# Performance work log

Hardware: AMD Instinct MI355X
Metric: run time of the kernel (lower is better)

## Reference

```python
import jax, jax.numpy as jnp
import numpy as np
import math

D_MODEL = 1024
N_HEADS = 16
D_HEAD = D_MODEL // N_HEADS
EPS = 1e-5


def layer_norm(x, w, b):
    mu = jnp.mean(x, axis=-1, keepdims=True)
    var = jnp.mean(jnp.square(x - mu), axis=-1, keepdims=True)
    return (x - mu) * jax.lax.rsqrt(var + EPS) * w + b


def setup_inputs() -> dict:
    key = jax.random.key(0)
    ks = jax.random.split(key, 8)
    b, n, d = 1, 4096, D_MODEL
    s = 0.02
    return {
        "x": jax.random.normal(ks[0], (b, n, d), dtype=jnp.float32),
        "ln1_w": jnp.ones((d,), jnp.float32),
        "ln1_b": jnp.zeros((d,), jnp.float32),
        "ln2_w": jnp.ones((d,), jnp.float32),
        "ln2_b": jnp.zeros((d,), jnp.float32),
        "w_qkv": jax.random.normal(ks[1], (d, 3 * d), jnp.float32) * s,  # [in, out]
        "w_o": jax.random.normal(ks[2], (d, d), jnp.float32) * s,
        "w_ff1": jax.random.normal(ks[3], (d, 4 * d), jnp.float32) * s,
        "b_ff1": jnp.zeros((4 * d,), jnp.float32),
        "w_ff2": jax.random.normal(ks[4], (4 * d, d), jnp.float32) * s,
        "b_ff2": jnp.zeros((d,), jnp.float32),
    }


def reference(x, ln1_w, ln1_b, ln2_w, ln2_b, w_qkv, w_o, w_ff1, b_ff1, w_ff2, b_ff2):
    b, n, d = x.shape
    # --- attention sub-block ---
    h = layer_norm(x, ln1_w, ln1_b)
    qkv = (h @ w_qkv).reshape(b, n, 3, N_HEADS, D_HEAD)
    q, k, v = qkv[:, :, 0], qkv[:, :, 1], qkv[:, :, 2]  # [b, n, h, dh]
    scale = 1.0 / math.sqrt(D_HEAD)
    s = jnp.einsum("bqhd,bkhd->bhqk", q, k) * scale  # materialized [b,h,n,n]
    causal = jnp.tril(jnp.ones((n, n), dtype=bool))
    s = jnp.where(causal, s, -jnp.inf)
    a = jax.nn.softmax(s, axis=-1)
    out = jnp.einsum("bhqk,bkhd->bqhd", a, v).reshape(b, n, d)
    x = x + out @ w_o
    # --- FFN sub-block ---
    h2 = layer_norm(x, ln2_w, ln2_b)
    ff = jax.nn.gelu(h2 @ w_ff1 + b_ff1, approximate=False) @ w_ff2 + b_ff2
    return x + ff
```

## Files before the change

kernel.cpp:

```cpp
#include <hip/hip_runtime.h>
#include <hip/hip_bf16.h>
#include <cstdint>
#include <cstddef>

typedef __attribute__((ext_vector_type(8))) __bf16 bf16x8;
typedef __attribute__((ext_vector_type(4))) __bf16 bf16x4;
typedef __attribute__((ext_vector_type(4))) float f32x4;
typedef __attribute__((ext_vector_type(16))) float f32x16;
typedef __attribute__((ext_vector_type(4))) unsigned int uint4v;

#define MFMA16(a, b, c) __builtin_amdgcn_mfma_f32_16x16x32_bf16(a, b, c, 0, 0, 0)
#define MFMA32(a, b, c) __builtin_amdgcn_mfma_f32_32x32x16_bf16(a, b, c, 0, 0, 0)

__device__ __forceinline__ void gload_lds16(const void* g, void* l) {
  __builtin_amdgcn_global_load_lds(
      (__attribute__((address_space(1))) uint32_t*)g,
      (__attribute__((address_space(3))) uint32_t*)l,
      16, 0, 0);
}

__device__ __forceinline__ unsigned pkbf(float a, float b) {
  unsigned short x = __builtin_bit_cast(unsigned short, (__bf16)a);
  unsigned short y = __builtin_bit_cast(unsigned short, (__bf16)b);
  return (unsigned)x | ((unsigned)y << 16);
}

__global__ __launch_bounds__(256) void transpose_all_kernel(
    const float* __restrict__ w_qkv, __bf16* __restrict__ wqkvT,
    const float* __restrict__ w_o, __bf16* __restrict__ woT,
    const float* __restrict__ w_ff1, __bf16* __restrict__ wff1T,
    const float* __restrict__ w_ff2, __bf16* __restrict__ wff2T) {
  __shared__ float tile[32][33];
  int bid = blockIdx.x;
  const float* in; __bf16* out; int K, N, bx, by;
  if (bid < 3072)      { in = w_qkv; out = wqkvT; K = 1024; N = 3072; bx = bid % 96;  by = bid / 96; }
  else if (bid < 4096) { int b = bid - 3072; in = w_o;   out = woT;   K = 1024; N = 1024; bx = b % 32;  by = b / 32; }
  else if (bid < 8192) { int b = bid - 4096; in = w_ff1; out = wff1T; K = 1024; N = 4096; bx = b % 128; by = b / 128; }
  else                 { int b = bid - 8192; in = w_ff2; out = wff2T; K = 4096; N = 1024; bx = b % 32;  by = b / 32; }
  int tx = threadIdx.x, ty = threadIdx.y;
  int gcol = bx * 32 + tx;
#pragma unroll
  for (int j = 0; j < 4; j++) {
    int grow = by * 32 + ty + j * 8;
    tile[ty + j * 8][tx] = in[(size_t)grow * N + gcol];
  }
  __syncthreads();
#pragma unroll
  for (int j = 0; j < 4; j++) {
    int n = bx * 32 + ty + j * 8;
    out[(size_t)n * K + by * 32 + tx] = (__bf16)tile[tx][ty + j * 8];
  }
}

__global__ __launch_bounds__(256) void ln_kernel(
    const float* __restrict__ x, const float* __restrict__ w,
    const float* __restrict__ b, __bf16* __restrict__ out) {
  int row = blockIdx.x;
  int t = threadIdx.x;
  const float4* xr = (const float4*)(x + (size_t)row * 1024);
  float4 v = xr[t];
  float s = v.x + v.y + v.z + v.w;
  float sq = v.x * v.x + v.y * v.y + v.z * v.z + v.w * v.w;
#pragma unroll
  for (int m = 1; m < 64; m <<= 1) {
    s += __shfl_xor(s, m);
    sq += __shfl_xor(sq, m);
  }
  __shared__ float rs[4], rq[4];
  int wid = t >> 6;
  if ((t & 63) == 0) { rs[wid] = s; rq[wid] = sq; }
  __syncthreads();
  s = rs[0] + rs[1] + rs[2] + rs[3];
  sq = rq[0] + rq[1] + rq[2] + rq[3];
  float mean = s * (1.0f / 1024.0f);
  float var = sq * (1.0f / 1024.0f) - mean * mean;
  float rstd = rsqrtf(var + 1e-5f);
  int c = t * 4;
  float4 wv = ((const float4*)w)[t];
  float4 bv = ((const float4*)b)[t];
  bf16x4 o;
  o[0] = (__bf16)((v.x - mean) * rstd * wv.x + bv.x);
  o[1] = (__bf16)((v.y - mean) * rstd * wv.y + bv.y);
  o[2] = (__bf16)((v.z - mean) * rstd * wv.z + bv.z);
  o[3] = (__bf16)((v.w - mean) * rstd * wv.w + bv.w);
  *(bf16x4*)(out + (size_t)row * 1024 + c) = o;
}

template <int EPI>
__global__ __launch_bounds__(256, 2) void gemm_kernel(
    const __bf16* __restrict__ A, const __bf16* __restrict__ BT,
    int M, int N, int K,
    const float* __restrict__ resid, const float* __restrict__ bias,
    float* __restrict__ outf, __bf16* __restrict__ outb) {
  __shared__ __bf16 lsA[128 * 64];
  __shared__ __bf16 lsB[128 * 64];
  int t = threadIdx.x;
  int m0 = blockIdx.y * 128, n0 = blockIdx.x * 128;
  int wid = t >> 6, lane = t & 63, lo = lane & 15, g = lane >> 4;
  int wr = wid >> 1, wc = wid & 1;
  f32x4 acc[4][4] = {};
  const __bf16* ag = A + (size_t)(m0 + (t >> 3)) * K + (t & 7) * 8;
  const __bf16* bg = BT + (size_t)(n0 + (t >> 3)) * K + (t & 7) * 8;
  for (int k0 = 0; k0 < K; k0 += 64) {
#pragma unroll
    for (int i = 0; i < 4; i++) {
      gload_lds16(ag + (size_t)i * 32 * K + k0, &lsA[i * 2048 + t * 8]);
      gload_lds16(bg + (size_t)i * 32 * K + k0, &lsB[i * 2048 + t * 8]);
    }
    __syncthreads();
#pragma unroll
    for (int kk = 0; kk < 2; kk++) {
      bf16x8 af[4], bfr[4];
#pragma unroll
      for (int mi = 0; mi < 4; mi++)
        af[mi] = *(const bf16x8*)&lsA[(wr * 64 + mi * 16 + lo) * 64 + kk * 32 + g * 8];
#pragma unroll
      for (int ni = 0; ni < 4; ni++)
        bfr[ni] = *(const bf16x8*)&lsB[(wc * 64 + ni * 16 + lo) * 64 + kk * 32 + g * 8];
#pragma unroll
      for (int mi = 0; mi < 4; mi++)
#pragma unroll
        for (int ni = 0; ni < 4; ni++)
          acc[mi][ni] = MFMA16(af[mi], bfr[ni], acc[mi][ni]);
    }
    __syncthreads();
  }
#pragma unroll
  for (int mi = 0; mi < 4; mi++) {
#pragma unroll
    for (int ni = 0; ni < 4; ni++) {
      int col = n0 + wc * 64 + ni * 16 + lo;
      int row0 = m0 + wr * 64 + mi * 16 + g * 4;
#pragma unroll
      for (int r = 0; r < 4; r++) {
        int row = row0 + r;
        float val = acc[mi][ni][r];
        size_t idx = (size_t)row * N + col;
        outf[idx] = resid[idx] + val;
      }
    }
  }
}

template <int EPI>
__global__ __launch_bounds__(512, 2) void gemm256_kernel(
    const __bf16* __restrict__ A, const __bf16* __restrict__ BT,
    int M, int N, int K, int nkc,
    const float* __restrict__ bias, __bf16* __restrict__ outb,
    __bf16* __restrict__ P0, __bf16* __restrict__ P1,
    __bf16* __restrict__ P2, __bf16* __restrict__ P3) {
  __shared__ __bf16 lsA[2][2][128 * 64];
  __shared__ __bf16 lsB[2][2][128 * 64];
  int nbx = N >> 8;
  int nwg = (M >> 8) * nbx;
  int bid = blockIdx.x;
  int swz = (bid & 7) * (nwg >> 3) + (bid >> 3);
  int m0 = (swz / nbx) << 8, n0 = (swz % nbx) << 8;
  int kc = blockIdx.y;
  int kt0 = kc * nkc;
  int t = threadIdx.x;
  int wid = t >> 6, lane = t & 63, lo = lane & 15, g = lane >> 4;
  int wm = wid >> 2, wn = wid & 3;
  int srow = t >> 3, sgrp = t & 7;

  auto stA = [&](int d, int h, int kt) {
#pragma unroll
    for (int i = 0; i < 2; i++) {
      int row = i * 64 + srow;
      int gs = (sgrp ^ (row & 7)) * 8;
      gload_lds16(A + (size_t)(m0 + h * 128 + row) * K + kt * 64 + gs,
                  &lsA[d][h][(i * 512 + t) * 8]);
    }
  };
  auto stB = [&](int d, int h, int kt) {
#pragma unroll
    for (int i = 0; i < 2; i++) {
      int row = i * 64 + srow;
      int gs = (sgrp ^ (row & 7)) * 8;
      gload_lds16(BT + (size_t)(n0 + h * 128 + row) * K + kt * 64 + gs,
                  &lsB[d][h][(i * 512 + t) * 8]);
    }
  };
  auto rdA = [&](int d, int f, int kk) -> bf16x8 {
    int row = (f & 3) * 32 + wm * 16 + lo;
    return *(const bf16x8*)&lsA[d][f >> 2][row * 64 + (((kk * 4 + g) ^ (lo & 7)) * 8)];
  };
  auto rdB = [&](int d, int ni, int kk) -> bf16x8 {
    int row = (ni & 1) * 64 + wn * 16 + lo;
    return *(const bf16x8*)&lsB[d][ni >> 1][row * 64 + (((kk * 4 + g) ^ (lo & 7)) * 8)];
  };

  f32x4 acc[8][4] = {};
  stA(0, 0, kt0); stB(0, 0, kt0); stB(0, 1, kt0); stA(0, 1, kt0);
  asm volatile("s_waitcnt vmcnt(4)" ::: "memory");
  __builtin_amdgcn_s_barrier();

  for (int ki = 0; ki < nkc; ki++) {
    int kt = kt0 + ki;
    int d = ki & 1, nx = d ^ 1;
    bool pf = (ki + 1) < nkc;
    bf16x8 fa[4][2], fb0[2][2], fb1[2][2];
#pragma unroll
    for (int f = 0; f < 4; f++) { fa[f][0] = rdA(d, f, 0); fa[f][1] = rdA(d, f, 1); }
#pragma unroll
    for (int n = 0; n < 2; n++) { fb0[n][0] = rdB(d, n, 0); fb0[n][1] = rdB(d, n, 1); }
    if (pf) { stA(nx, 0, kt + 1); stB(nx, 0, kt + 1); }
    __builtin_amdgcn_s_barrier();
    __builtin_amdgcn_s_setprio(1);
#pragma unroll
    for (int f = 0; f < 4; f++)
#pragma unroll
      for (int n = 0; n < 2; n++) {
        acc[f][n] = MFMA16(fa[f][0], fb0[n][0], acc[f][n]);
        acc[f][n] = MFMA16(fa[f][1], fb0[n][1], acc[f][n]);
      }
    __builtin_amdgcn_s_setprio(0);
    asm volatile("s_waitcnt vmcnt(6)" ::: "memory");
    __builtin_amdgcn_s_barrier();
#pragma unroll
    for (int n = 0; n < 2; n++) { fb1[n][0] = rdB(d, 2 + n, 0); fb1[n][1] = rdB(d, 2 + n, 1); }
    if (pf) stB(nx, 1, kt + 1);
    __builtin_amdgcn_s_barrier();
    __builtin_amdgcn_s_setprio(1);
#pragma unroll
    for (int f = 0; f < 4; f++)
#pragma unroll
      for (int n = 0; n < 2; n++) {
        acc[f][2 + n] = MFMA16(fa[f][0], fb1[n][0], acc[f][2 + n]);
        acc[f][2 + n] = MFMA16(fa[f][1], fb1[n][1], acc[f][2 + n]);
      }
    __builtin_amdgcn_s_setprio(0);
    asm volatile("s_waitcnt vmcnt(6)" ::: "memory");
    __builtin_amdgcn_s_barrier();
#pragma unroll
    for (int f = 0; f < 4; f++) { fa[f][0] = rdA(d, 4 + f, 0); fa[f][1] = rdA(d, 4 + f, 1); }
    if (pf) stA(nx, 1, kt + 1);
    __builtin_amdgcn_s_barrier();
    __builtin_amdgcn_s_setprio(1);
#pragma unroll
    for (int f = 0; f < 4; f++)
#pragma unroll
      for (int n = 0; n < 2; n++) {
        acc[4 + f][2 + n] = MFMA16(fa[f][0], fb1[n][0], acc[4 + f][2 + n]);
        acc[4 + f][2 + n] = MFMA16(fa[f][1], fb1[n][1], acc[4 + f][2 + n]);
      }
    __builtin_amdgcn_s_setprio(0);
    __builtin_amdgcn_s_barrier();
    __builtin_amdgcn_s_setprio(1);
#pragma unroll
    for (int f = 0; f < 4; f++)
#pragma unroll
      for (int n = 0; n < 2; n++) {
        acc[4 + f][n] = MFMA16(fa[f][0], fb0[n][0], acc[4 + f][n]);
        acc[4 + f][n] = MFMA16(fa[f][1], fb0[n][1], acc[4 + f][n]);
      }
    __builtin_amdgcn_s_setprio(0);
    asm volatile("s_waitcnt vmcnt(4)" ::: "memory");
    __builtin_amdgcn_s_barrier();
  }

  __bf16* pk = (EPI == 4) ? ((kc == 0) ? P0 : (kc == 1) ? P1 : (kc == 2) ? P2 : P3)
                          : nullptr;
#pragma unroll
  for (int f = 0; f < 8; f++) {
    int row0 = m0 + (f >> 2) * 128 + (f & 3) * 32 + wm * 16 + g * 4;
#pragma unroll
    for (int ni = 0; ni < 4; ni++) {
      int col = n0 + (ni >> 1) * 128 + (ni & 1) * 64 + wn * 16 + lo;
      if (EPI == 0) {
        int sE = col >> 10, rem = col & 1023, hh = rem >> 6, dd = rem & 63;
        if (sE < 2) {
          float qs = (sE == 0) ? 0.1803368801111204f : 1.0f;
#pragma unroll
          for (int r = 0; r < 4; r++)
            outb[((size_t)(sE * 16 + hh) * 4096 + row0 + r) * 64 + dd] =
                (__bf16)(acc[f][ni][r] * qs);
        } else {
          bf16x4 pk4;
#pragma unroll
          for (int r = 0; r < 4; r++) pk4[r] = (__bf16)acc[f][ni][r];
          *(bf16x4*)&outb[(size_t)32 * 4096 * 64 + ((size_t)(hh * 64 + dd)) * 4096 + row0] = pk4;
        }
      } else if (EPI == 2) {
        float bv = bias[col];
#pragma unroll
        for (int r = 0; r < 4; r++) {
          float vv = acc[f][ni][r] + bv;
          float gg = 0.5f * vv * (1.0f + erff(vv * 0.70710678118f));
          outb[(size_t)(row0 + r) * N + col] = (__bf16)gg;
        }
      } else {
#pragma unroll
        for (int r = 0; r < 4; r++)
          pk[(size_t)(row0 + r) * N + col] = (__bf16)acc[f][ni][r];
      }
    }
  }
}

__global__ __launch_bounds__(256) void ff2_reduce_kernel(
    const __bf16* __restrict__ p0, const __bf16* __restrict__ p1,
    const __bf16* __restrict__ p2, const __bf16* __restrict__ p3,
    const float* __restrict__ x2, const float* __restrict__ bias,
    float* __restrict__ out) {
  size_t i8 = ((size_t)blockIdx.x * 256 + threadIdx.x) * 8;
  bf16x8 a = *(const bf16x8*)&p0[i8];
  bf16x8 b = *(const bf16x8*)&p1[i8];
  bf16x8 c = *(const bf16x8*)&p2[i8];
  bf16x8 d = *(const bf16x8*)&p3[i8];
  int col = (int)(i8 & 1023);
  float4 xa = *(const float4*)&x2[i8];
  float4 xb = *(const float4*)&x2[i8 + 4];
  float4 ba = *(const float4*)&bias[col];
  float4 bb = *(const float4*)&bias[col + 4];
  float4 oa, ob;
  oa.x = xa.x + ba.x + (float)a[0] + (float)b[0] + (float)c[0] + (float)d[0];
  oa.y = xa.y + ba.y + (float)a[1] + (float)b[1] + (float)c[1] + (float)d[1];
  oa.z = xa.z + ba.z + (float)a[2] + (float)b[2] + (float)c[2] + (float)d[2];
  oa.w = xa.w + ba.w + (float)a[3] + (float)b[3] + (float)c[3] + (float)d[3];
  ob.x = xb.x + bb.x + (float)a[4] + (float)b[4] + (float)c[4] + (float)d[4];
  ob.y = xb.y + bb.y + (float)a[5] + (float)b[5] + (float)c[5] + (float)d[5];
  ob.z = xb.z + bb.z + (float)a[6] + (float)b[6] + (float)c[6] + (float)d[6];
  ob.w = xb.w + bb.w + (float)a[7] + (float)b[7] + (float)c[7] + (float)d[7];
  *(float4*)&out[i8] = oa;
  *(float4*)&out[i8 + 4] = ob;
}

__global__ __launch_bounds__(512, 4) void attn_kernel(
    const __bf16* __restrict__ Q, const __bf16* __restrict__ Kb,
    const __bf16* __restrict__ VTb, __bf16* __restrict__ O) {
  constexpr int NSEQ = 4096;
  __shared__ __bf16 lds[2][2][2][64 * 64];
  int orig = blockIdx.x;
  int xcd = orig & 7, rank = orig >> 3;
  int hv = rank >> 5;
  int hd2 = (rank >> 4) & 1;
  int itr = rank & 15;
  int head = xcd * 2 + hd2;
  int it = hv ? itr : (31 - itr);
  int t = threadIdx.x, wid = t >> 6, lane = t & 63;
  int lo = lane & 31, hi = lane >> 5;
  int qsub = wid & 3, kpar = wid >> 2;
  const __bf16* kh = Kb + (size_t)head * NSEQ * 64;
  const __bf16* vth = VTb + (size_t)head * 64 * NSEQ;
  int qlow = it * 128 + qsub * 32;
  int qrow = qlow + lo;
  const __bf16* qh = Q + (size_t)head * NSEQ * 64 + (size_t)qrow * 64;
  bf16x8 bq[4];
#pragma unroll
  for (int c = 0; c < 4; c++) bq[c] = *(const bf16x8*)(qh + c * 16 + hi * 8);

  const unsigned onesu = 0x3F803F80u;
  uint4v onev = {onesu, onesu, onesu, onesu};
  bf16x8 vones = __builtin_bit_cast(bf16x8, onev);

  f32x16 acc0 = {}, acc1 = {};
  f32x16 lacc = {};
  int srow = t >> 3;
  int sgs = ((t & 7) ^ (srow & 7)) * 8;

  auto stage_tile = [&](int d, int par, int kt) {
    gload_lds16(kh + (size_t)(kt * 64 + srow) * 64 + sgs, &lds[d][par][0][t * 8]);
    gload_lds16(vth + (size_t)srow * NSEQ + kt * 64 + sgs, &lds[d][par][1][t * 8]);
  };

  int ns = it + 1;
  stage_tile(0, 0, 0);
  stage_tile(0, 1, 1);
  __syncthreads();
  for (int j = 0; j < ns; j++) {
    int cur = j & 1;
    if (j + 1 < ns) {
      stage_tile(cur ^ 1, 0, 2 * j + 2);
      stage_tile(cur ^ 1, 1, 2 * j + 3);
    }
    int kt = 2 * j + kpar;
    if (kt * 64 <= qlow + 31) {
      const __bf16* lk = lds[cur][kpar][0];
      const __bf16* lvt = lds[cur][kpar][1];
      f32x16 s0 = {}, s1 = {};
      __builtin_amdgcn_s_setprio(1);
#pragma unroll
      for (int c = 0; c < 4; c++) {
        bf16x8 ka0 = *(const bf16x8*)&lk[(size_t)lo * 64 + (((c * 2 + hi) ^ (lo & 7)) * 8)];
        bf16x8 ka1 = *(const bf16x8*)&lk[(size_t)(32 + lo) * 64 + (((c * 2 + hi) ^ (lo & 7)) * 8)];
        s0 = MFMA32(ka0, bq[c], s0);
        s1 = MFMA32(ka1, bq[c], s1);
      }
      __builtin_amdgcn_s_setprio(0);
      if (kt * 64 + 63 > qlow) {
#pragma unroll
        for (int i = 0; i < 16; i++) {
          int key0 = kt * 64 + (i & 3) + 8 * (i >> 2) + 4 * hi;
          if (key0 > qrow) s0[i] = -3.0e38f;
          if (key0 + 32 > qrow) s1[i] = -3.0e38f;
        }
      }
#pragma unroll
      for (int i = 0; i < 16; i++) {
        s0[i] = exp2f(s0[i]);
        s1[i] = exp2f(s1[i]);
      }
      uint4v pw[4];
#pragma unroll
      for (int b = 0; b < 2; b++) {
        int off = b * 8;
        unsigned a0 = pkbf(s0[off + 0], s0[off + 1]);
        unsigned a1 = pkbf(s0[off + 2], s0[off + 3]);
        unsigned b0 = pkbf(s0[off + 4], s0[off + 5]);
        unsigned b1 = pkbf(s0[off + 6], s0[off + 7]);
        asm("v_permlane32_swap_b32 %0, %1" : "+v"(a0), "+v"(b0));
        asm("v_permlane32_swap_b32 %0, %1" : "+v"(a1), "+v"(b1));
        pw[b][0] = a0; pw[b][1] = a1; pw[b][2] = b0; pw[b][3] = b1;
        unsigned c0 = pkbf(s1[off + 0], s1[off + 1]);
        unsigned c1 = pkbf(s1[off + 2], s1[off + 3]);
        unsigned d0 = pkbf(s1[off + 4], s1[off + 5]);
        unsigned d1 = pkbf(s1[off + 6], s1[off + 7]);
        asm("v_permlane32_swap_b32 %0, %1" : "+v"(c0), "+v"(d0));
        asm("v_permlane32_swap_b32 %0, %1" : "+v"(c1), "+v"(d1));
        pw[2 + b][0] = c0; pw[2 + b][1] = c1; pw[2 + b][2] = d0; pw[2 + b][3] = d1;
      }
      __builtin_amdgcn_s_setprio(1);
#pragma unroll
      for (int b = 0; b < 4; b++) {
        bf16x8 pf = __builtin_bit_cast(bf16x8, pw[b]);
        bf16x8 va0 = *(const bf16x8*)&lvt[(size_t)lo * 64 + (((b * 2 + hi) ^ (lo & 7)) * 8)];
        bf16x8 va1 = *(const bf16x8*)&lvt[(size_t)(32 + lo) * 64 + (((b * 2 + hi) ^ (lo & 7)) * 8)];
        acc0 = MFMA32(va0, pf, acc0);
        acc1 = MFMA32(va1, pf, acc1);
        lacc = MFMA32(vones, pf, lacc);
      }
      __builtin_amdgcn_s_setprio(0);
    }
    __syncthreads();
  }
  float* fl = (float*)lds;
  float* lbuf = fl;
  float* ab = fl + 256;
  __bf16* bounce = (__bf16*)(fl + 256 + 9216);
  if (kpar == 1) {
    lbuf[qsub * 64 + lane] = lacc[0];
    int base = (qsub * 64 + lane) * 36;
#pragma unroll
    for (int k2 = 0; k2 < 16; k2 += 4) {
      float4 v0; v0.x = acc0[k2]; v0.y = acc0[k2 + 1]; v0.z = acc0[k2 + 2]; v0.w = acc0[k2 + 3];
      *(float4*)&ab[base + k2] = v0;
      float4 v1; v1.x = acc1[k2]; v1.y = acc1[k2 + 1]; v1.z = acc1[k2 + 2]; v1.w = acc1[k2 + 3];
      *(float4*)&ab[base + 16 + k2] = v1;
    }
  }
  __syncthreads();
  if (kpar == 0) {
    float lsum = lacc[0] + lbuf[qsub * 64 + lane];
    float linv = 1.0f / lsum;
    int base = (qsub * 64 + lane) * 36;
    f32x16 b0, b1;
#pragma unroll
    for (int k2 = 0; k2 < 16; k2 += 4) {
      float4 v0 = *(float4*)&ab[base + k2];
      b0[k2] = v0.x; b0[k2 + 1] = v0.y; b0[k2 + 2] = v0.z; b0[k2 + 3] = v0.w;
      float4 v1 = *(float4*)&ab[base + 16 + k2];
      b1[k2] = v1.x; b1[k2 + 1] = v1.y; b1[k2 + 2] = v1.z; b1[k2 + 3] = v1.w;
    }
    __bf16* region = bounce + qsub * 2048;
#pragma unroll
    for (int dt = 0; dt < 2; dt++) {
#pragma unroll
      for (int rp = 0; rp < 8; rp++) {
        int r = rp * 2;
        float a0 = dt ? acc1[r] : acc0[r], a1 = dt ? acc1[r + 1] : acc0[r + 1];
        float c0 = dt ? b1[r] : b0[r], c1 = dt ? b1[r + 1] : b0[r + 1];
        float e0 = (a0 + c0) * linv;
        float e1 = (a1 + c1) * linv;
        int d = dt * 32 + (r & 3) + 8 * (r >> 2) + 4 * hi;
        int bytecol = d * 2;
        int g16 = bytecol >> 4, rem16 = bytecol & 15;
        *(unsigned*)((char*)region + lo * 128 + ((g16 ^ (lo & 7)) * 16 + rem16)) = pkbf(e0, e1);
      }
    }
#pragma unroll
    for (int j2 = 0; j2 < 4; j2++) {
      int idx = j2 * 64 + lane;
      int row = idx >> 3, g = idx & 7;
      bf16x8 v = *(const bf16x8*)((char*)region + row * 128 + ((g ^ (row & 7)) * 16));
      *(bf16x8*)&O[(size_t)(it * 128 + qsub * 32 + row) * 1024 + head * 64 + g * 8] = v;
    }
  }
}

extern "C" void kernel_launch(void* const* d_in, const int* in_sizes, int n_in,
                              void* d_out, int out_size, void* d_ws, size_t ws_size,
                              hipStream_t stream) {
  const float* x = (const float*)d_in[0];
  const float* ln1_w = (const float*)d_in[1];
  const float* ln1_b = (const float*)d_in[2];
  const float* ln2_w = (const float*)d_in[3];
  const float* ln2_b = (const float*)d_in[4];
  const float* w_qkv = (const float*)d_in[5];
  const float* w_o = (const float*)d_in[6];
  const float* w_ff1 = (const float*)d_in[7];
  const float* b_ff1 = (const float*)d_in[8];
  const float* w_ff2 = (const float*)d_in[9];
  const float* b_ff2 = (const float*)d_in[10];
  float* out = (float*)d_out;

  const size_t D = 1024, NT = 4096;
  __bf16* wqkvT = (__bf16*)d_ws;
  __bf16* woT = wqkvT + 3072 * D;
  __bf16* wff1T = woT + D * D;
  __bf16* wff2T = wff1T + 4096 * D;
  __bf16* hbuf = wff2T + D * 4096;
  __bf16* qkvb = hbuf + NT * D;
  __bf16* attnb = qkvb + 3 * NT * D;
  __bf16* a1 = qkvb;
  float* x2 = (float*)(attnb + NT * D);
  __bf16* p0 = (__bf16*)d_ws;
  __bf16* p1 = p0 + NT * D;
  __bf16* p2 = hbuf;
  __bf16* p3 = (__bf16*)(x2 + NT * D);

  dim3 tb(32, 8);
  transpose_all_kernel<<<12288, tb, 0, stream>>>(w_qkv, wqkvT, w_o, woT,
                                                 w_ff1, wff1T, w_ff2, wff2T);

  ln_kernel<<<4096, 256, 0, stream>>>(x, ln1_w, ln1_b, hbuf);
  gemm256_kernel<0><<<192, 512, 0, stream>>>(hbuf, wqkvT, 4096, 3072, 1024, 16,
                                             nullptr, qkvb, nullptr, nullptr, nullptr, nullptr);
  attn_kernel<<<512, 512, 0, stream>>>(
      qkvb, qkvb + 16 * NT * 64, qkvb + 32 * NT * 64, attnb);
  gemm_kernel<1><<<dim3(1024 / 128, 4096 / 128), 256, 0, stream>>>(
      attnb, woT, 4096, 1024, 1024, x, nullptr, x2, nullptr);
  ln_kernel<<<4096, 256, 0, stream>>>(x2, ln2_w, ln2_b, hbuf);
  gemm256_kernel<2><<<256, 512, 0, stream>>>(hbuf, wff1T, 4096, 4096, 1024, 16,
                                             b_ff1, a1, nullptr, nullptr, nullptr, nullptr);
  gemm256_kernel<4><<<dim3(64, 4), 512, 0, stream>>>(a1, wff2T, 4096, 1024, 4096, 16,
                                                     nullptr, nullptr, p0, p1, p2, p3);
  ff2_reduce_kernel<<<2048, 256, 0, stream>>>(p0, p1, p2, p3, x2, b_ff2, out);
}
```

Baseline: 247.8 us.

## Split-K the output projection GEMM and unroll attention loop by buffer parity

The output projection GEMM now splits K in two across blockIdx.z, which doubles the workgroup count from 256 to 512. Each half writes bf16 partials into the reused qkv buffer, and a new reduce kernel adds them together with the residual. Separately, the attention main loop is unrolled by two so the double-buffer index becomes a compile-time constant, and the LDS offsets and staging addresses are precomputed outside the loop. The split adds an extra kernel launch, the partial write and read traffic, and bf16 rounding of the partial sums.

```diff
diff --git a/kernel.cpp b/kernel.cpp
--- a/kernel.cpp
+++ b/kernel.cpp
@@ -86,22 +86,21 @@
   *(bf16x4*)(out + (size_t)row * 1024 + c) = o;
 }
 
-template <int EPI>
-__global__ __launch_bounds__(256, 2) void gemm_kernel(
+__global__ __launch_bounds__(256, 2) void gemm_splitk128_kernel(
     const __bf16* __restrict__ A, const __bf16* __restrict__ BT,
-    int M, int N, int K,
-    const float* __restrict__ resid, const float* __restrict__ bias,
-    float* __restrict__ outf, __bf16* __restrict__ outb) {
+    int M, int N, int K, int kchunk, __bf16* __restrict__ P) {
   __shared__ __bf16 lsA[128 * 64];
   __shared__ __bf16 lsB[128 * 64];
   int t = threadIdx.x;
   int m0 = blockIdx.y * 128, n0 = blockIdx.x * 128;
+  int kbase = blockIdx.z * kchunk;
+  __bf16* pout = P + (size_t)blockIdx.z * M * N;
   int wid = t >> 6, lane = t & 63, lo = lane & 15, g = lane >> 4;
   int wr = wid >> 1, wc = wid & 1;
   f32x4 acc[4][4] = {};
   const __bf16* ag = A + (size_t)(m0 + (t >> 3)) * K + (t & 7) * 8;
   const __bf16* bg = BT + (size_t)(n0 + (t >> 3)) * K + (t & 7) * 8;
-  for (int k0 = 0; k0 < K; k0 += 64) {
+  for (int k0 = kbase; k0 < kbase + kchunk; k0 += 64) {
 #pragma unroll
     for (int i = 0; i < 4; i++) {
       gload_lds16(ag + (size_t)i * 32 * K + k0, &lsA[i * 2048 + t * 8]);
@@ -132,14 +131,31 @@
       int col = n0 + wc * 64 + ni * 16 + lo;
       int row0 = m0 + wr * 64 + mi * 16 + g * 4;
 #pragma unroll
-      for (int r = 0; r < 4; r++) {
-        int row = row0 + r;
-        float val = acc[mi][ni][r];
-        size_t idx = (size_t)row * N + col;
-        outf[idx] = resid[idx] + val;
-      }
-    }
-  }
+      for (int r = 0; r < 4; r++)
+        pout[(size_t)(row0 + r) * N + col] = (__bf16)acc[mi][ni][r];
+    }
+  }
+}
+
+__global__ __launch_bounds__(256) void out_reduce2_kernel(
+    const __bf16* __restrict__ p0, const __bf16* __restrict__ p1,
+    const float* __restrict__ x, float* __restrict__ out) {
+  size_t i8 = ((size_t)blockIdx.x * 256 + threadIdx.x) * 8;
+  bf16x8 a = *(const bf16x8*)&p0[i8];
+  bf16x8 b = *(const bf16x8*)&p1[i8];
+  float4 xa = *(const float4*)&x[i8];
+  float4 xb = *(const float4*)&x[i8 + 4];
+  float4 oa, ob;
+  oa.x = xa.x + (float)a[0] + (float)b[0];
+  oa.y = xa.y + (float)a[1] + (float)b[1];
+  oa.z = xa.z + (float)a[2] + (float)b[2];
+  oa.w = xa.w + (float)a[3] + (float)b[3];
+  ob.x = xb.x + (float)a[4] + (float)b[4];
+  ob.y = xb.y + (float)a[5] + (float)b[5];
+  ob.z = xb.z + (float)a[6] + (float)b[6];
+  ob.w = xb.w + (float)a[7] + (float)b[7];
+  *(float4*)&out[i8] = oa;
+  *(float4*)&out[i8 + 4] = ob;
 }
 
 template <int EPI>
@@ -359,81 +375,99 @@
   int srow = t >> 3;
   int sgs = ((t & 7) ^ (srow & 7)) * 8;
 
+  int off[4];
+#pragma unroll
+  for (int c = 0; c < 4; c++) off[c] = lo * 64 + (((c * 2 + hi) ^ (lo & 7)) * 8);
+  const __bf16* lk0 = &lds[0][kpar][0][0];
+  const __bf16* lk1 = &lds[1][kpar][0][0];
+  const __bf16* lv0 = &lds[0][kpar][1][0];
+  const __bf16* lv1 = &lds[1][kpar][1][0];
+  const __bf16* khs = kh + srow * 64 + sgs;
+  const __bf16* vts = vth + (size_t)srow * NSEQ + sgs;
+
   auto stage_tile = [&](int d, int par, int kt) {
-    gload_lds16(kh + (size_t)(kt * 64 + srow) * 64 + sgs, &lds[d][par][0][t * 8]);
-    gload_lds16(vth + (size_t)srow * NSEQ + kt * 64 + sgs, &lds[d][par][1][t * 8]);
+    gload_lds16(khs + (size_t)kt * 4096, &lds[d][par][0][t * 8]);
+    gload_lds16(vts + kt * 64, &lds[d][par][1][t * 8]);
   };
 
   int ns = it + 1;
+  int qtop = qlow + 31;
   stage_tile(0, 0, 0);
   stage_tile(0, 1, 1);
   __syncthreads();
-  for (int j = 0; j < ns; j++) {
-    int cur = j & 1;
-    if (j + 1 < ns) {
-      stage_tile(cur ^ 1, 0, 2 * j + 2);
-      stage_tile(cur ^ 1, 1, 2 * j + 3);
-    }
-    int kt = 2 * j + kpar;
-    if (kt * 64 <= qlow + 31) {
-      const __bf16* lk = lds[cur][kpar][0];
-      const __bf16* lvt = lds[cur][kpar][1];
-      f32x16 s0 = {}, s1 = {};
-      __builtin_amdgcn_s_setprio(1);
-#pragma unroll
-      for (int c = 0; c < 4; c++) {
-        bf16x8 ka0 = *(const bf16x8*)&lk[(size_t)lo * 64 + (((c * 2 + hi) ^ (lo & 7)) * 8)];
-        bf16x8 ka1 = *(const bf16x8*)&lk[(size_t)(32 + lo) * 64 + (((c * 2 + hi) ^ (lo & 7)) * 8)];
-        s0 = MFMA32(ka0, bq[c], s0);
-        s1 = MFMA32(ka1, bq[c], s1);
-      }
-      __builtin_amdgcn_s_setprio(0);
-      if (kt * 64 + 63 > qlow) {
-#pragma unroll
-        for (int i = 0; i < 16; i++) {
-          int key0 = kt * 64 + (i & 3) + 8 * (i >> 2) + 4 * hi;
-          if (key0 > qrow) s0[i] = -3.0e38f;
-          if (key0 + 32 > qrow) s1[i] = -3.0e38f;
-        }
-      }
-#pragma unroll
-      for (int i = 0; i < 16; i++) {
-        s0[i] = exp2f(s0[i]);
-        s1[i] = exp2f(s1[i]);
-      }
-      uint4v pw[4];
-#pragma unroll
-      for (int b = 0; b < 2; b++) {
-        int off = b * 8;
-        unsigned a0 = pkbf(s0[off + 0], s0[off + 1]);
-        unsigned a1 = pkbf(s0[off + 2], s0[off + 3]);
-        unsigned b0 = pkbf(s0[off + 4], s0[off + 5]);
-        unsigned b1 = pkbf(s0[off + 6], s0[off + 7]);
-        asm("v_permlane32_swap_b32 %0, %1" : "+v"(a0), "+v"(b0));
-        asm("v_permlane32_swap_b32 %0, %1" : "+v"(a1), "+v"(b1));
-        pw[b][0] = a0; pw[b][1] = a1; pw[b][2] = b0; pw[b][3] = b1;
-        unsigned c0 = pkbf(s1[off + 0], s1[off + 1]);
-        unsigned c1 = pkbf(s1[off + 2], s1[off + 3]);
-        unsigned d0 = pkbf(s1[off + 4], s1[off + 5]);
-        unsigned d1 = pkbf(s1[off + 6], s1[off + 7]);
-        asm("v_permlane32_swap_b32 %0, %1" : "+v"(c0), "+v"(d0));
-        asm("v_permlane32_swap_b32 %0, %1" : "+v"(c1), "+v"(d1));
-        pw[2 + b][0] = c0; pw[2 + b][1] = c1; pw[2 + b][2] = d0; pw[2 + b][3] = d1;
-      }
-      __builtin_amdgcn_s_setprio(1);
-#pragma unroll
-      for (int b = 0; b < 4; b++) {
-        bf16x8 pf = __builtin_bit_cast(bf16x8, pw[b]);
-        bf16x8 va0 = *(const bf16x8*)&lvt[(size_t)lo * 64 + (((b * 2 + hi) ^ (lo & 7)) * 8)];
-        bf16x8 va1 = *(const bf16x8*)&lvt[(size_t)(32 + lo) * 64 + (((b * 2 + hi) ^ (lo & 7)) * 8)];
-        acc0 = MFMA32(va0, pf, acc0);
-        acc1 = MFMA32(va1, pf, acc1);
-        lacc = MFMA32(vones, pf, lacc);
-      }
-      __builtin_amdgcn_s_setprio(0);
-    }
-    __syncthreads();
-  }
+
+#define ATTN_STEP(CUR)                                                         \
+  {                                                                            \
+    if (j + 1 < ns) {                                                          \
+      stage_tile((CUR) ^ 1, 0, 2 * j + 2);                                     \
+      stage_tile((CUR) ^ 1, 1, 2 * j + 3);                                     \
+    }                                                                          \
+    int kt = 2 * j + kpar;                                                     \
+    if (kt * 64 <= qtop) {                                                     \
+      const __bf16* lk = (CUR) ? lk1 : lk0;                                    \
+      const __bf16* lvt = (CUR) ? lv1 : lv0;                                   \
+      f32x16 s0 = {}, s1 = {};                                                 \
+      __builtin_amdgcn_s_setprio(1);                                           \
+      _Pragma("unroll") for (int c = 0; c < 4; c++) {                          \
+        bf16x8 ka0 = *(const bf16x8*)&lk[off[c]];                              \
+        bf16x8 ka1 = *(const bf16x8*)&lk[2048 + off[c]];                       \
+        s0 = MFMA32(ka0, bq[c], s0);                                           \
+        s1 = MFMA32(ka1, bq[c], s1);                                           \
+      }                                                                        \
+      __builtin_amdgcn_s_setprio(0);                                           \
+      if (kt * 64 + 63 > qlow) {                                               \
+        _Pragma("unroll") for (int i = 0; i < 16; i++) {                       \
+          int key0 = kt * 64 + (i & 3) + 8 * (i >> 2) + 4 * hi;                \
+          if (key0 > qrow) s0[i] = -3.0e38f;                                   \
+          if (key0 + 32 > qrow) s1[i] = -3.0e38f;                              \
+        }                                                                      \
+      }                                                                        \
+      _Pragma("unroll") for (int i = 0; i < 16; i++) {                         \
+        s0[i] = exp2f(s0[i]);                                                  \
+        s1[i] = exp2f(s1[i]);                                                  \
+      }                                                                        \
+      uint4v pw[4];                                                            \
+      _Pragma("unroll") for (int b = 0; b < 2; b++) {                          \
+        int off2 = b * 8;                                                      \
+        unsigned a0 = pkbf(s0[off2 + 0], s0[off2 + 1]);                        \
+        unsigned a1 = pkbf(s0[off2 + 2], s0[off2 + 3]);                        \
+        unsigned b0 = pkbf(s0[off2 + 4], s0[off2 + 5]);                        \
+        unsigned b1 = pkbf(s0[off2 + 6], s0[off2 + 7]);                        \
+        asm("v_permlane32_swap_b32 %0, %1" : "+v"(a0), "+v"(b0));              \
+        asm("v_permlane32_swap_b32 %0, %1" : "+v"(a1), "+v"(b1));              \
+        pw[b][0] = a0; pw[b][1] = a1; pw[b][2] = b0; pw[b][3] = b1;            \
+        unsigned c0 = pkbf(s1[off2 + 0], s1[off2 + 1]);                        \
+        unsigned c1 = pkbf(s1[off2 + 2], s1[off2 + 3]);                        \
+        unsigned d0 = pkbf(s1[off2 + 4], s1[off2 + 5]);                        \
+        unsigned d1 = pkbf(s1[off2 + 6], s1[off2 + 7]);                        \
+        asm("v_permlane32_swap_b32 %0, %1" : "+v"(c0), "+v"(d0));              \
+        asm("v_permlane32_swap_b32 %0, %1" : "+v"(c1), "+v"(d1));              \
+        pw[2 + b][0] = c0; pw[2 + b][1] = c1; pw[2 + b][2] = d0;               \
+        pw[2 + b][3] = d1;                                                     \
+      }                                                                        \
+      __builtin_amdgcn_s_setprio(1);                                           \
+      _Pragma("unroll") for (int b = 0; b < 4; b++) {                          \
+        bf16x8 pf = __builtin_bit_cast(bf16x8, pw[b]);                         \
+        bf16x8 va0 = *(const bf16x8*)&lvt[off[b]];                             \
+        bf16x8 va1 = *(const bf16x8*)&lvt[2048 + off[b]];                      \
+        acc0 = MFMA32(va0, pf, acc0);                                          \
+        acc1 = MFMA32(va1, pf, acc1);                                          \
+        lacc = MFMA32(vones, pf, lacc);                                        \
+      }                                                                        \
+      __builtin_amdgcn_s_setprio(0);                                           \
+    }                                                                          \
+    __syncthreads();                                                           \
+  }
+
+  int j = 0;
+  for (;;) {
+    ATTN_STEP(0);
+    if (++j >= ns) break;
+    ATTN_STEP(1);
+    if (++j >= ns) break;
+  }
+#undef ATTN_STEP
+
   float* fl = (float*)lds;
   float* lbuf = fl;
   float* ab = fl + 256;
@@ -518,6 +552,8 @@
   __bf16* p1 = p0 + NT * D;
   __bf16* p2 = hbuf;
   __bf16* p3 = (__bf16*)(x2 + NT * D);
+  __bf16* pA = qkvb;
+  __bf16* pB = pA + NT * D;
 
   dim3 tb(32, 8);
   transpose_all_kernel<<<12288, tb, 0, stream>>>(w_qkv, wqkvT, w_o, woT,
@@ -528,8 +564,9 @@
                                              nullptr, qkvb, nullptr, nullptr, nullptr, nullptr);
   attn_kernel<<<512, 512, 0, stream>>>(
       qkvb, qkvb + 16 * NT * 64, qkvb + 32 * NT * 64, attnb);
-  gemm_kernel<1><<<dim3(1024 / 128, 4096 / 128), 256, 0, stream>>>(
-      attnb, woT, 4096, 1024, 1024, x, nullptr, x2, nullptr);
+  gemm_splitk128_kernel<<<dim3(8, 32, 2), 256, 0, stream>>>(
+      attnb, woT, 4096, 1024, 1024, 512, pA);
+  out_reduce2_kernel<<<2048, 256, 0, stream>>>(pA, pB, x, x2);
   ln_kernel<<<4096, 256, 0, stream>>>(x2, ln2_w, ln2_b, hbuf);
   gemm256_kernel<2><<<256, 512, 0, stream>>>(hbuf, wff1T, 4096, 4096, 1024, 16,
                                              b_ff1, a1, nullptr, nullptr, nullptr, nullptr);
```

Result: no change. 246.4 us (-0.6%).
